# Optimization experiments

Hardware: AMD Instinct MI355X
Metric: run time of the kernel (lower is better)

## Reference

```python
import jax, jax.numpy as jnp
import numpy as np

NUM_HEADS = 12
HEAD_DIM = 64
MAX_POS = 1024  # max_position_embeddings


def setup_inputs() -> dict:
    key = jax.random.key(0)
    ks = jax.random.split(key, 6)
    B, S, H = 4, 1024, 768
    return {
        "hidden_states": jax.random.normal(ks[0], (B, S, H), dtype=jnp.float32),
        "attention_mask": jnp.zeros((B, 1, 1, S), dtype=jnp.float32),
        "Wq": jax.random.normal(ks[1], (H, H), dtype=jnp.float32) * 0.02,
        "bq": jnp.zeros((H,), dtype=jnp.float32),
        "Wk": jax.random.normal(ks[2], (H, H), dtype=jnp.float32) * 0.02,
        "bk": jnp.zeros((H,), dtype=jnp.float32),
        "Wv": jax.random.normal(ks[3], (H, H), dtype=jnp.float32) * 0.02,
        "bv": jnp.zeros((H,), dtype=jnp.float32),
        "dist_emb": jax.random.normal(ks[4], (2 * MAX_POS - 1, HEAD_DIM), dtype=jnp.float32) * 0.02,
    }


def _split_heads(x):
    # [B, S, H] -> [B, nh, S, hd]
    B, S, _ = x.shape
    return x.reshape(B, S, NUM_HEADS, HEAD_DIM).transpose(0, 2, 1, 3)


def reference(hidden_states, attention_mask, Wq, bq, Wk, bk, Wv, bv, dist_emb):
    B, S, H = hidden_states.shape
    q = _split_heads(hidden_states @ Wq + bq)  # [B, nh, S, hd]
    k = _split_heads(hidden_states @ Wk + bk)
    v = _split_heads(hidden_states @ Wv + bv)

    # raw scores QK^T: [B, nh, S, S]
    scores = jnp.einsum("bhld,bhrd->bhlr", q, k)

    # relative_key_query positional bias
    dist = jnp.arange(S)[:, None] - jnp.arange(S)[None, :] + MAX_POS - 1  # [S, S]
    pos = dist_emb[dist]  # [S, S, hd]
    scores = scores + jnp.einsum("bhld,lrd->bhlr", q, pos) \
                    + jnp.einsum("bhrd,lrd->bhlr", k, pos)

    scores = scores / jnp.sqrt(jnp.asarray(HEAD_DIM, scores.dtype))
    scores = scores + attention_mask  # additive mask broadcast [B,1,1,S]

    probs = jax.nn.softmax(scores, axis=-1)  # dropout prob = 0.0 (eval)
    ctx = jnp.einsum("bhlr,bhrd->bhld", probs, v)  # [B, nh, S, hd]
    ctx = ctx.transpose(0, 2, 1, 3).reshape(B, S, H)
    return ctx
```

## Files before the change

kernel.cpp:

```cpp
#include <hip/hip_runtime.h>

#define SEQ 1024
#define NH  12
#define HD  64
#define HID 768
#define NB  4

#define LOG2E  1.4426950408889634f
#define SC2    0.18033688011112042f
#define DTHR   11.541560327111707f

typedef short bf16x8 __attribute__((ext_vector_type(8)));
typedef float f32x16 __attribute__((ext_vector_type(16)));

__device__ __forceinline__ unsigned short f2b(float f) {
    union { float f; unsigned u; } v; v.f = f;
    unsigned r = (v.u + 0x7FFFu + ((v.u >> 16) & 1u)) >> 16;
    return (unsigned short)r;
}
__device__ __forceinline__ float b2f(unsigned short s) {
    union { unsigned u; float f; } v; v.u = (unsigned)s << 16;
    return v.f;
}
__device__ __forceinline__ float g4(const float4& v, int e) {
    return e == 0 ? v.x : e == 1 ? v.y : e == 2 ? v.z : v.w;
}

#define ROWFN(r, h) (((r) & 3) + 8 * ((r) >> 2) + 4 * (h))

__global__ void cvt_bf16(const float* __restrict__ in, unsigned short* __restrict__ outp, int n4) {
    int i = blockIdx.x * blockDim.x + threadIdx.x;
    const int stride = gridDim.x * blockDim.x;
    for (; i < n4; i += stride) {
        float4 v = ((const float4*)in)[i];
        ushort4 o;
        o.x = f2b(v.x); o.y = f2b(v.y); o.z = f2b(v.z); o.w = f2b(v.w);
        ((ushort4*)outp)[i] = o;
    }
}

__global__ __launch_bounds__(256) void cvt_wt(
    const float* __restrict__ Wq, const float* __restrict__ Wk, const float* __restrict__ Wv,
    unsigned short* __restrict__ Wt)
{
    __shared__ float T[64][65];
    const int z = blockIdx.z;
    const float* __restrict__ W = (z == 0) ? Wq : (z == 1) ? Wk : Wv;
    const int k0 = blockIdx.x * 64, n0 = blockIdx.y * 64;
    const int tid = threadIdx.x;
    #pragma unroll
    for (int ir = 0; ir < 4; ++ir) {
        int r = ir * 16 + (tid >> 4);
        int c4 = (tid & 15) * 4;
        *(float4*)&T[r][c4] = *(const float4*)&W[(size_t)(k0 + r) * HID + n0 + c4];
    }
    __syncthreads();
    const int cc = tid >> 2, q = tid & 3;
    unsigned short* dst = Wt + (size_t)z * HID * HID + (size_t)(n0 + cc) * HID + k0 + q * 16;
    #pragma unroll
    for (int j4 = 0; j4 < 4; ++j4) {
        ushort4 t4;
        t4.x = f2b(T[q * 16 + j4 * 4 + 0][cc]);
        t4.y = f2b(T[q * 16 + j4 * 4 + 1][cc]);
        t4.z = f2b(T[q * 16 + j4 * 4 + 2][cc]);
        t4.w = f2b(T[q * 16 + j4 * 4 + 3][cc]);
        *(ushort4*)(dst + j4 * 4) = t4;
    }
}

__global__ __launch_bounds__(256) void gemm_qkv(
    const unsigned short* __restrict__ Xb,
    const unsigned short* __restrict__ Wt,
    const float* __restrict__ bq, const float* __restrict__ bk, const float* __restrict__ bv,
    unsigned short* __restrict__ qkv)
{
    __shared__ unsigned short Xs[128][64];
    __shared__ unsigned short Ws[128][64];

    const int tid = threadIdx.x;
    const int lane = tid & 63;
    const int wid = tid >> 6;
    const int c = lane & 31;
    const int h2 = lane >> 5;
    const int m0 = blockIdx.x * 128, N0 = blockIdx.y * 128, z = blockIdx.z;
    const unsigned short* __restrict__ Wz = Wt + (size_t)z * HID * HID;
    const float* __restrict__ bias = (z == 0) ? bq : (z == 1) ? bk : bv;

    f32x16 acc[2][2];
    #pragma unroll
    for (int i = 0; i < 2; ++i)
        #pragma unroll
        for (int j = 0; j < 2; ++j)
            #pragma unroll
            for (int r = 0; r < 16; ++r) acc[i][j][r] = 0.f;

    for (int k0 = 0; k0 < HID; k0 += 64) {
        __syncthreads();
        #pragma unroll
        for (int it = 0; it < 4; ++it) {
            int t16 = tid + 256 * it;
            int row = t16 >> 3, s = t16 & 7;
            bf16x8 xv = *(const bf16x8*)(Xb + (size_t)(m0 + row) * HID + k0 + s * 8);
            *(bf16x8*)&Xs[row][(s ^ (row & 7)) * 8] = xv;
            bf16x8 wv = *(const bf16x8*)(Wz + (size_t)(N0 + row) * HID + k0 + s * 8);
            *(bf16x8*)&Ws[row][(s ^ (row & 7)) * 8] = wv;
        }
        __syncthreads();
        #pragma unroll
        for (int kc = 0; kc < 4; ++kc) {
            const int slot = kc * 2 + h2;
            bf16x8 af[2], bf_[2];
            #pragma unroll
            for (int i = 0; i < 2; ++i) {
                int ar = 64 * (wid >> 1) + 32 * i + c;
                int br = 64 * (wid & 1) + 32 * i + c;
                if (z != 2) {
                    af[i]  = *(const bf16x8*)&Xs[ar][(slot ^ (ar & 7)) * 8];
                    bf_[i] = *(const bf16x8*)&Ws[br][(slot ^ (br & 7)) * 8];
                } else {
                    af[i]  = *(const bf16x8*)&Ws[ar][(slot ^ (ar & 7)) * 8];
                    bf_[i] = *(const bf16x8*)&Xs[br][(slot ^ (br & 7)) * 8];
                }
            }
            #pragma unroll
            for (int i = 0; i < 2; ++i)
                #pragma unroll
                for (int j = 0; j < 2; ++j)
                    acc[i][j] = __builtin_amdgcn_mfma_f32_32x32x16_bf16(af[i], bf_[j], acc[i][j], 0, 0, 0);
        }
    }

    unsigned short* outz = qkv + (size_t)z * (NB * SEQ * HID);
    if (z != 2) {
        #pragma unroll
        for (int j = 0; j < 2; ++j) {
            const int n = N0 + 64 * (wid & 1) + 32 * j + c;
            const float bv_ = bias[n];
            const int hh = n >> 6, d = n & 63;
            #pragma unroll
            for (int i = 0; i < 2; ++i) {
                #pragma unroll
                for (int r = 0; r < 16; ++r) {
                    int m = m0 + 64 * (wid >> 1) + 32 * i + ROWFN(r, h2);
                    int bb = m >> 10, ss = m & 1023;
                    outz[(((size_t)bb * NH + hh) * SEQ + ss) * HD + d] = f2b(acc[i][j][r] + bv_);
                }
            }
        }
    } else {
        #pragma unroll
        for (int i = 0; i < 2; ++i) {
            #pragma unroll
            for (int r = 0; r < 16; ++r) {
                int n = N0 + 64 * (wid >> 1) + 32 * i + ROWFN(r, h2);
                float bv_ = bias[n];
                int hh = n >> 6, d = n & 63;
                #pragma unroll
                for (int j = 0; j < 2; ++j) {
                    int m = m0 + 64 * (wid & 1) + 32 * j + c;
                    int bb = m >> 10, ss = m & 1023;
                    outz[(((size_t)bb * NH + hh) * HD + d) * SEQ + ss] = f2b(acc[i][j][r] + bv_);
                }
            }
        }
    }
}

struct PF { bf16x8 kb[4], ka[4], e0[4], e1[4], v0, v1; };

__global__ __launch_bounds__(256, 2) void attn_mfma(
    const unsigned short* __restrict__ Qg,
    const unsigned short* __restrict__ Kg,
    const unsigned short* __restrict__ Vtg,
    const unsigned short* __restrict__ Eg,
    const float* __restrict__ mask,
    float* __restrict__ out)
{
    __shared__ unsigned short Vt[2][64][64];
    __shared__ float S1T[64 * 64];
    __shared__ unsigned short Mt[128][68];
    __shared__ unsigned short Nt[128][68];
    __shared__ unsigned short Pl[64][64];
    __shared__ float Corr[64];
    __shared__ float InvL[64];

    const int tid = threadIdx.x;
    const int lane = tid & 63;
    const int wid = tid >> 6;
    const int c = lane & 31;
    const int h2 = lane >> 5;
    const int RB = 32 * (wid >> 1);
    const int CB = 32 * (wid & 1);

    const int l0 = blockIdx.x * 64;
    const int bh = blockIdx.y;
    const int b = bh / NH;
    const int hh = bh - b * NH;

    const unsigned short* __restrict__ Qb = Qg + (size_t)bh * SEQ * HD;
    const unsigned short* __restrict__ Kb = Kg + (size_t)bh * SEQ * HD;
    const unsigned short* __restrict__ Vb = Vtg + (size_t)bh * HD * SEQ;
    const float* __restrict__ mrow_base = mask + (size_t)b * SEQ;

    bf16x8 qa[4];
    #pragma unroll
    for (int kc = 0; kc < 4; ++kc)
        qa[kc] = *(const bf16x8*)(Qb + (size_t)(l0 + RB + c) * HD + kc * 16 + h2 * 8);

    f32x16 Oa;
    #pragma unroll
    for (int r = 0; r < 16; ++r) Oa[r] = 0.f;

    const int li = tid >> 2;
    const int c0q = (tid & 3) * 16;
    const int kli = (li ^ (li >> 3)) & 7;
    const int vd0 = tid >> 3, vs8 = tid & 7;
    float m_run = -1e30f, lsum = 0.f;

    PF P;
    {
        const int jb = l0 + 960;
        const int jr0 = jb + 64 * (wid & 1) + c;
        #pragma unroll
        for (int kc = 0; kc < 4; ++kc) {
            P.kb[kc] = *(const bf16x8*)(Kb + (size_t)(CB + c) * HD + kc * 16 + h2 * 8);
            P.ka[kc] = *(const bf16x8*)(Kb + (size_t)(RB + c) * HD + kc * 16 + h2 * 8);
            int jra = jr0 > 2046 ? 2046 : jr0;
            int jr1 = jr0 + 32; int jrb = jr1 > 2046 ? 2046 : jr1;
            P.e0[kc] = *(const bf16x8*)(Eg + (size_t)jra * HD + kc * 16 + h2 * 8);
            P.e1[kc] = *(const bf16x8*)(Eg + (size_t)jrb * HD + kc * 16 + h2 * 8);
        }
        P.v0 = *(const bf16x8*)(Vb + (size_t)vd0 * SEQ + vs8 * 8);
        P.v1 = *(const bf16x8*)(Vb + (size_t)(vd0 + 32) * SEQ + vs8 * 8);
    }

    for (int r0 = 0; r0 < SEQ; r0 += 64) {
        const int buf = (r0 >> 6) & 1;

        {
            const int kd0 = (vd0 ^ (vd0 >> 3)) & 7;
            *(bf16x8*)&Vt[buf][vd0][(vs8 ^ kd0) * 8] = P.v0;
            const int d1 = vd0 + 32;
            const int kd1 = (d1 ^ (d1 >> 3)) & 7;
            *(bf16x8*)&Vt[buf][d1][(vs8 ^ kd1) * 8] = P.v1;
        }

        f32x16 s1a, ma0, na0;
        #pragma unroll
        for (int r = 0; r < 16; ++r) { s1a[r] = 0.f; ma0[r] = 0.f; na0[r] = 0.f; }
        __builtin_amdgcn_s_setprio(1);
        #pragma unroll
        for (int kc = 0; kc < 4; ++kc) {
            s1a = __builtin_amdgcn_mfma_f32_32x32x16_bf16(qa[kc], P.kb[kc], s1a, 0, 0, 0);
            ma0 = __builtin_amdgcn_mfma_f32_32x32x16_bf16(qa[kc], P.e0[kc], ma0, 0, 0, 0);
            na0 = __builtin_amdgcn_mfma_f32_32x32x16_bf16(P.ka[kc], P.e0[kc], na0, 0, 0, 0);
        }
        __builtin_amdgcn_s_setprio(0);
        {
            const int rcol = CB + c;
            #pragma unroll
            for (int q = 0; q < 4; ++q) {
                const int chunk = (RB >> 2) + 2 * q + h2;
                const int swz = chunk ^ (rcol & 15);
                float4 w4 = make_float4(s1a[4 * q + 0], s1a[4 * q + 1], s1a[4 * q + 2], s1a[4 * q + 3]);
                *(float4*)&S1T[rcol * 64 + swz * 4] = w4;
            }
        }
        {
            const int jc0 = 64 * (wid & 1) + c;
            #pragma unroll
            for (int q = 0; q < 4; ++q) {
                const int lb = RB + 8 * q + 4 * h2;
                ushort4 mw, nw;
                mw.x = f2b(ma0[4 * q + 0]); mw.y = f2b(ma0[4 * q + 1]);
                mw.z = f2b(ma0[4 * q + 2]); mw.w = f2b(ma0[4 * q + 3]);
                nw.x = f2b(na0[4 * q + 0]); nw.y = f2b(na0[4 * q + 1]);
                nw.z = f2b(na0[4 * q + 2]); nw.w = f2b(na0[4 * q + 3]);
                *(ushort4*)&Mt[jc0][lb] = mw;
                *(ushort4*)&Nt[jc0][lb] = nw;
            }
        }
        f32x16 ma1, na1;
        #pragma unroll
        for (int r = 0; r < 16; ++r) { ma1[r] = 0.f; na1[r] = 0.f; }
        __builtin_amdgcn_s_setprio(1);
        #pragma unroll
        for (int kc = 0; kc < 4; ++kc) {
            ma1 = __builtin_amdgcn_mfma_f32_32x32x16_bf16(qa[kc], P.e1[kc], ma1, 0, 0, 0);
            na1 = __builtin_amdgcn_mfma_f32_32x32x16_bf16(P.ka[kc], P.e1[kc], na1, 0, 0, 0);
        }
        __builtin_amdgcn_s_setprio(0);
        {
            const int jc1 = 64 * (wid & 1) + c + 32;
            #pragma unroll
            for (int q = 0; q < 4; ++q) {
                const int lb = RB + 8 * q + 4 * h2;
                ushort4 mw, nw;
                mw.x = f2b(ma1[4 * q + 0]); mw.y = f2b(ma1[4 * q + 1]);
                mw.z = f2b(ma1[4 * q + 2]); mw.w = f2b(ma1[4 * q + 3]);
                nw.x = f2b(na1[4 * q + 0]); nw.y = f2b(na1[4 * q + 1]);
                nw.z = f2b(na1[4 * q + 2]); nw.w = f2b(na1[4 * q + 3]);
                *(ushort4*)&Mt[jc1][lb] = mw;
                *(ushort4*)&Nt[jc1][lb] = nw;
            }
        }

        {
            int r0n = r0 + 64; if (r0n >= SEQ) r0n = 0;
            const int jb = l0 - r0n + 960;
            const int jr0 = jb + 64 * (wid & 1) + c;
            #pragma unroll
            for (int kc = 0; kc < 4; ++kc) {
                P.kb[kc] = *(const bf16x8*)(Kb + (size_t)(r0n + CB + c) * HD + kc * 16 + h2 * 8);
                P.ka[kc] = *(const bf16x8*)(Kb + (size_t)(r0n + RB + c) * HD + kc * 16 + h2 * 8);
                int jra = jr0 > 2046 ? 2046 : jr0;
                int jr1 = jr0 + 32; int jrb = jr1 > 2046 ? 2046 : jr1;
                P.e0[kc] = *(const bf16x8*)(Eg + (size_t)jra * HD + kc * 16 + h2 * 8);
                P.e1[kc] = *(const bf16x8*)(Eg + (size_t)jrb * HD + kc * 16 + h2 * 8);
            }
            P.v0 = *(const bf16x8*)(Vb + (size_t)vd0 * SEQ + r0n + vs8 * 8);
            P.v1 = *(const bf16x8*)(Vb + (size_t)(vd0 + 32) * SEQ + r0n + vs8 * 8);
        }

        __syncthreads();

        float4 mk[4];
        #pragma unroll
        for (int q = 0; q < 4; ++q)
            mk[q] = *(const float4*)(mrow_base + r0 + c0q + 4 * q);

        float sc[16];
        #pragma unroll
        for (int j = 0; j < 16; ++j) {
            const int rr = c0q + j;
            const int jdx = li - rr + 63;
            float s1v = S1T[rr * 64 + (((li >> 2) ^ j) << 2) + (li & 3)];
            float mv = b2f(Mt[jdx][li]);
            float nv = b2f(Nt[jdx][rr]);
            sc[j] = (s1v + mv + nv) * SC2 + g4(mk[j >> 2], j & 3) * LOG2E;
        }
        float tmax = sc[0];
        #pragma unroll
        for (int j = 1; j < 16; ++j) tmax = fmaxf(tmax, sc[j]);
        tmax = fmaxf(tmax, __shfl_xor(tmax, 1));
        tmax = fmaxf(tmax, __shfl_xor(tmax, 2));
        const bool upd = tmax > m_run + DTHR;
        const float m_new = upd ? tmax : m_run;
        const float corr = upd ? __builtin_amdgcn_exp2f(m_run - m_new) : 1.0f;
        float tsum = 0.f;
        unsigned short pb[16];
        #pragma unroll
        for (int j = 0; j < 16; ++j) {
            float p = __builtin_amdgcn_exp2f(sc[j] - m_new);
            tsum += p;
            pb[j] = f2b(p);
        }
        tsum += __shfl_xor(tsum, 1);
        tsum += __shfl_xor(tsum, 2);
        lsum = lsum * corr + tsum;
        m_run = m_new;
        if ((tid & 3) == 0) Corr[li] = corr;
        #pragma unroll
        for (int sblk = 0; sblk < 2; ++sblk) {
            bf16x8 pv;
            #pragma unroll
            for (int e = 0; e < 8; ++e) pv[e] = (short)pb[sblk * 8 + e];
            const int slot = ((c0q >> 3) + sblk) ^ kli;
            *(bf16x8*)&Pl[li][slot * 8] = pv;
        }

        __syncthreads();

        #pragma unroll
        for (int q = 0; q < 4; ++q) {
            float4 cr = *(const float4*)&Corr[RB + 8 * q + 4 * h2];
            Oa[4 * q + 0] *= cr.x; Oa[4 * q + 1] *= cr.y;
            Oa[4 * q + 2] *= cr.z; Oa[4 * q + 3] *= cr.w;
        }
        const int lrow = RB + c;
        const int drow = CB + c;
        const int klr = (lrow ^ (lrow >> 3)) & 7;
        const int kdr = (drow ^ (drow >> 3)) & 7;
        __builtin_amdgcn_s_setprio(1);
        #pragma unroll
        for (int kc = 0; kc < 4; ++kc) {
            const int slot = kc * 2 + h2;
            bf16x8 pa  = *(const bf16x8*)&Pl[lrow][(slot ^ klr) * 8];
            bf16x8 vbf = *(const bf16x8*)&Vt[buf][drow][(slot ^ kdr) * 8];
            Oa = __builtin_amdgcn_mfma_f32_32x32x16_bf16(pa, vbf, Oa, 0, 0, 0);
        }
        __builtin_amdgcn_s_setprio(0);
    }

    if ((tid & 3) == 0) InvL[li] = 1.0f / lsum;
    __syncthreads();
    #pragma unroll
    for (int q = 0; q < 4; ++q) {
        float4 iv = *(const float4*)&InvL[RB + 8 * q + 4 * h2];
        #pragma unroll
        for (int e = 0; e < 4; ++e) {
            const int l = RB + 8 * q + 4 * h2 + e;
            out[((size_t)b * SEQ + l0 + l) * HID + hh * HD + CB + c] = Oa[4 * q + e] * g4(iv, e);
        }
    }
}

extern "C" void kernel_launch(void* const* d_in, const int* in_sizes, int n_in,
                              void* d_out, int out_size, void* d_ws, size_t ws_size,
                              hipStream_t stream) {
    const float* hidden = (const float*)d_in[0];
    const float* mask   = (const float*)d_in[1];
    const float* Wq     = (const float*)d_in[2];
    const float* bq     = (const float*)d_in[3];
    const float* Wk     = (const float*)d_in[4];
    const float* bk     = (const float*)d_in[5];
    const float* Wv     = (const float*)d_in[6];
    const float* bv     = (const float*)d_in[7];
    const float* E      = (const float*)d_in[8];
    float* outp = (float*)d_out;

    unsigned short* ws  = (unsigned short*)d_ws;
    unsigned short* Xbf = ws;
    unsigned short* Wt  = ws + 3145728;
    unsigned short* Ebf = ws + 4915200;
    unsigned short* qkv = ws + 5046272;

    cvt_bf16<<<dim3(1024), 256, 0, stream>>>(hidden, Xbf, 786432);
    cvt_bf16<<<dim3(128),  256, 0, stream>>>(E, Ebf, 32752);
    cvt_wt<<<dim3(12, 12, 3), 256, 0, stream>>>(Wq, Wk, Wv, Wt);
    gemm_qkv<<<dim3(32, 6, 3), 256, 0, stream>>>(Xbf, Wt, bq, bk, bv, qkv);
    const size_t per = (size_t)NB * SEQ * HID;
    attn_mfma<<<dim3(16, 48), 256, 0, stream>>>(qkv, qkv + per, qkv + 2 * per,
                                                Ebf, mask, outp);
}
```

Baseline: 187.1 us.

## Pre-skew relative-position tiles in LDS and single-buffer V to raise occupancy

The M and N positional bias tiles are now scattered at write time into per-row skewed layouts (MSS, NST), and S1 is stored row-major. The softmax phase can then read contiguous float4/ushort4 vectors instead of gathering 16 scalars through diagonal indexing. V is single-buffered in LDS, written after the barrier from registers carried over from the previous iteration, and launch bounds move to three blocks per CU. This cuts LDS footprint and the cost of the softmax-phase reads. In exchange it adds predicated scalar LDS stores in the score-write phase and more register pressure under the tighter bound.

```diff
diff --git a/kernel.cpp b/kernel.cpp
--- a/kernel.cpp
+++ b/kernel.cpp
@@ -23,6 +23,9 @@
     return v.f;
 }
 __device__ __forceinline__ float g4(const float4& v, int e) {
+    return e == 0 ? v.x : e == 1 ? v.y : e == 2 ? v.z : v.w;
+}
+__device__ __forceinline__ unsigned short u16g(const ushort4& v, int e) {
     return e == 0 ? v.x : e == 1 ? v.y : e == 2 ? v.z : v.w;
 }
 
@@ -166,9 +169,9 @@
     }
 }
 
-struct PF { bf16x8 kb[4], ka[4], e0[4], e1[4], v0, v1; };
-
-__global__ __launch_bounds__(256, 2) void attn_mfma(
+struct PF { bf16x8 kb[4], ka[4], e0[4], e1[4]; };
+
+__global__ __launch_bounds__(256, 3) void attn_mfma(
     const unsigned short* __restrict__ Qg,
     const unsigned short* __restrict__ Kg,
     const unsigned short* __restrict__ Vtg,
@@ -176,10 +179,10 @@
     const float* __restrict__ mask,
     float* __restrict__ out)
 {
-    __shared__ unsigned short Vt[2][64][64];
-    __shared__ float S1T[64 * 64];
-    __shared__ unsigned short Mt[128][68];
-    __shared__ unsigned short Nt[128][68];
+    __shared__ unsigned short Vt[64][64];
+    __shared__ float S1[64][68];
+    __shared__ unsigned short MSS[64][76];
+    __shared__ unsigned short NST[64][76];
     __shared__ unsigned short Pl[64][64];
     __shared__ float Corr[64];
     __shared__ float InvL[64];
@@ -191,6 +194,7 @@
     const int h2 = lane >> 5;
     const int RB = 32 * (wid >> 1);
     const int CB = 32 * (wid & 1);
+    const int j0 = 64 * (wid & 1) + c;
 
     const int l0 = blockIdx.x * 64;
     const int bh = blockIdx.y;
@@ -215,12 +219,14 @@
     const int c0q = (tid & 3) * 16;
     const int kli = (li ^ (li >> 3)) & 7;
     const int vd0 = tid >> 3, vs8 = tid & 7;
+    const int kd0 = (vd0 ^ (vd0 >> 3)) & 7;
+    const int kd1 = ((vd0 + 32) ^ ((vd0 + 32) >> 3)) & 7;
     float m_run = -1e30f, lsum = 0.f;
 
     PF P;
+    bf16x8 vc0, vc1;
     {
-        const int jb = l0 + 960;
-        const int jr0 = jb + 64 * (wid & 1) + c;
+        const int jr0 = l0 + 960 + j0;
         #pragma unroll
         for (int kc = 0; kc < 4; ++kc) {
             P.kb[kc] = *(const bf16x8*)(Kb + (size_t)(CB + c) * HD + kc * 16 + h2 * 8);
@@ -230,21 +236,11 @@
             P.e0[kc] = *(const bf16x8*)(Eg + (size_t)jra * HD + kc * 16 + h2 * 8);
             P.e1[kc] = *(const bf16x8*)(Eg + (size_t)jrb * HD + kc * 16 + h2 * 8);
         }
-        P.v0 = *(const bf16x8*)(Vb + (size_t)vd0 * SEQ + vs8 * 8);
-        P.v1 = *(const bf16x8*)(Vb + (size_t)(vd0 + 32) * SEQ + vs8 * 8);
+        vc0 = *(const bf16x8*)(Vb + (size_t)vd0 * SEQ + vs8 * 8);
+        vc1 = *(const bf16x8*)(Vb + (size_t)(vd0 + 32) * SEQ + vs8 * 8);
     }
 
     for (int r0 = 0; r0 < SEQ; r0 += 64) {
-        const int buf = (r0 >> 6) & 1;
-
-        {
-            const int kd0 = (vd0 ^ (vd0 >> 3)) & 7;
-            *(bf16x8*)&Vt[buf][vd0][(vs8 ^ kd0) * 8] = P.v0;
-            const int d1 = vd0 + 32;
-            const int kd1 = (d1 ^ (d1 >> 3)) & 7;
-            *(bf16x8*)&Vt[buf][d1][(vs8 ^ kd1) * 8] = P.v1;
-        }
-
         f32x16 s1a, ma0, na0;
         #pragma unroll
         for (int r = 0; r < 16; ++r) { s1a[r] = 0.f; ma0[r] = 0.f; na0[r] = 0.f; }
@@ -256,29 +252,16 @@
             na0 = __builtin_amdgcn_mfma_f32_32x32x16_bf16(P.ka[kc], P.e0[kc], na0, 0, 0, 0);
         }
         __builtin_amdgcn_s_setprio(0);
-        {
-            const int rcol = CB + c;
-            #pragma unroll
-            for (int q = 0; q < 4; ++q) {
-                const int chunk = (RB >> 2) + 2 * q + h2;
-                const int swz = chunk ^ (rcol & 15);
-                float4 w4 = make_float4(s1a[4 * q + 0], s1a[4 * q + 1], s1a[4 * q + 2], s1a[4 * q + 3]);
-                *(float4*)&S1T[rcol * 64 + swz * 4] = w4;
-            }
-        }
-        {
-            const int jc0 = 64 * (wid & 1) + c;
-            #pragma unroll
-            for (int q = 0; q < 4; ++q) {
-                const int lb = RB + 8 * q + 4 * h2;
-                ushort4 mw, nw;
-                mw.x = f2b(ma0[4 * q + 0]); mw.y = f2b(ma0[4 * q + 1]);
-                mw.z = f2b(ma0[4 * q + 2]); mw.w = f2b(ma0[4 * q + 3]);
-                nw.x = f2b(na0[4 * q + 0]); nw.y = f2b(na0[4 * q + 1]);
-                nw.z = f2b(na0[4 * q + 2]); nw.w = f2b(na0[4 * q + 3]);
-                *(ushort4*)&Mt[jc0][lb] = mw;
-                *(ushort4*)&Nt[jc0][lb] = nw;
-            }
+        #pragma unroll
+        for (int rq = 0; rq < 16; ++rq)
+            S1[RB + ROWFN(rq, h2)][CB + c] = s1a[rq];
+        #pragma unroll
+        for (int rq = 0; rq < 16; ++rq) {
+            const int lr = RB + ROWFN(rq, h2);
+            int rA = lr - j0 + 63;
+            if ((unsigned)rA < 64u) MSS[lr][rA] = f2b(ma0[rq]);
+            int lA = j0 + lr - 63;
+            if ((unsigned)lA < 64u) NST[lA][lr] = f2b(na0[rq]);
         }
         f32x16 ma1, na1;
         #pragma unroll
@@ -290,25 +273,19 @@
             na1 = __builtin_amdgcn_mfma_f32_32x32x16_bf16(P.ka[kc], P.e1[kc], na1, 0, 0, 0);
         }
         __builtin_amdgcn_s_setprio(0);
-        {
-            const int jc1 = 64 * (wid & 1) + c + 32;
-            #pragma unroll
-            for (int q = 0; q < 4; ++q) {
-                const int lb = RB + 8 * q + 4 * h2;
-                ushort4 mw, nw;
-                mw.x = f2b(ma1[4 * q + 0]); mw.y = f2b(ma1[4 * q + 1]);
-                mw.z = f2b(ma1[4 * q + 2]); mw.w = f2b(ma1[4 * q + 3]);
-                nw.x = f2b(na1[4 * q + 0]); nw.y = f2b(na1[4 * q + 1]);
-                nw.z = f2b(na1[4 * q + 2]); nw.w = f2b(na1[4 * q + 3]);
-                *(ushort4*)&Mt[jc1][lb] = mw;
-                *(ushort4*)&Nt[jc1][lb] = nw;
-            }
-        }
-
+        #pragma unroll
+        for (int rq = 0; rq < 16; ++rq) {
+            const int lr = RB + ROWFN(rq, h2);
+            int rB = lr - j0 + 31;
+            if ((unsigned)rB < 64u) MSS[lr][rB] = f2b(ma1[rq]);
+            int lB = j0 + lr - 31;
+            if ((unsigned)lB < 64u) NST[lB][lr] = f2b(na1[rq]);
+        }
+
+        bf16x8 vn0, vn1;
         {
             int r0n = r0 + 64; if (r0n >= SEQ) r0n = 0;
-            const int jb = l0 - r0n + 960;
-            const int jr0 = jb + 64 * (wid & 1) + c;
+            const int jr0 = l0 - r0n + 960 + j0;
             #pragma unroll
             for (int kc = 0; kc < 4; ++kc) {
                 P.kb[kc] = *(const bf16x8*)(Kb + (size_t)(r0n + CB + c) * HD + kc * 16 + h2 * 8);
@@ -318,26 +295,32 @@
                 P.e0[kc] = *(const bf16x8*)(Eg + (size_t)jra * HD + kc * 16 + h2 * 8);
                 P.e1[kc] = *(const bf16x8*)(Eg + (size_t)jrb * HD + kc * 16 + h2 * 8);
             }
-            P.v0 = *(const bf16x8*)(Vb + (size_t)vd0 * SEQ + r0n + vs8 * 8);
-            P.v1 = *(const bf16x8*)(Vb + (size_t)(vd0 + 32) * SEQ + r0n + vs8 * 8);
+            vn0 = *(const bf16x8*)(Vb + (size_t)vd0 * SEQ + r0n + vs8 * 8);
+            vn1 = *(const bf16x8*)(Vb + (size_t)(vd0 + 32) * SEQ + r0n + vs8 * 8);
         }
 
         __syncthreads();
+
+        *(bf16x8*)&Vt[vd0][(vs8 ^ kd0) * 8] = vc0;
+        *(bf16x8*)&Vt[vd0 + 32][(vs8 ^ kd1) * 8] = vc1;
 
         float4 mk[4];
         #pragma unroll
         for (int q = 0; q < 4; ++q)
             mk[q] = *(const float4*)(mrow_base + r0 + c0q + 4 * q);
-
+        float4 s4[4]; ushort4 mm[4], nn[4];
+        #pragma unroll
+        for (int q = 0; q < 4; ++q) {
+            s4[q] = *(const float4*)&S1[li][c0q + 4 * q];
+            mm[q] = *(const ushort4*)&MSS[li][c0q + 4 * q];
+            nn[q] = *(const ushort4*)&NST[li][c0q + 4 * q];
+        }
         float sc[16];
         #pragma unroll
         for (int j = 0; j < 16; ++j) {
-            const int rr = c0q + j;
-            const int jdx = li - rr + 63;
-            float s1v = S1T[rr * 64 + (((li >> 2) ^ j) << 2) + (li & 3)];
-            float mv = b2f(Mt[jdx][li]);
-            float nv = b2f(Nt[jdx][rr]);
-            sc[j] = (s1v + mv + nv) * SC2 + g4(mk[j >> 2], j & 3) * LOG2E;
+            float mv = b2f(u16g(mm[j >> 2], j & 3));
+            float nv = b2f(u16g(nn[j >> 2], j & 3));
+            sc[j] = (g4(s4[j >> 2], j & 3) + mv + nv) * SC2 + g4(mk[j >> 2], j & 3) * LOG2E;
         }
         float tmax = sc[0];
         #pragma unroll
@@ -386,10 +369,12 @@
         for (int kc = 0; kc < 4; ++kc) {
             const int slot = kc * 2 + h2;
             bf16x8 pa  = *(const bf16x8*)&Pl[lrow][(slot ^ klr) * 8];
-            bf16x8 vbf = *(const bf16x8*)&Vt[buf][drow][(slot ^ kdr) * 8];
+            bf16x8 vbf = *(const bf16x8*)&Vt[drow][(slot ^ kdr) * 8];
             Oa = __builtin_amdgcn_mfma_f32_32x32x16_bf16(pa, vbf, Oa, 0, 0, 0);
         }
         __builtin_amdgcn_s_setprio(0);
+
+        vc0 = vn0; vc1 = vn1;
     }
 
     if ((tid & 3) == 0) InvL[li] = 1.0f / lsum;
```

Result: slower. 403.0 us (+115.4%).
